# Kernel tuning notes

Hardware: AMD Instinct MI355X
Metric: run time of the kernel (lower is better)

The kernel has to match this reference:

```python
import jax, jax.numpy as jnp
import numpy as np

N, E, P = 50000, 1600000, 500000
IN_DIM, HID, OUT = 512, 128, 64
EPS = 1e-5


def setup_inputs() -> dict:
    key = jax.random.key(0)
    ks = jax.random.split(key, 16)
    d = {}
    d['x'] = jax.random.normal(ks[0], (N, IN_DIM), dtype=jnp.float32)
    d['ei'] = jax.random.randint(ks[1], (2, E), 0, N, dtype=jnp.int32)
    d['src'] = jax.random.randint(ks[2], (P,), 0, N, dtype=jnp.int32)
    d['dst'] = jax.random.randint(ks[3], (P,), 0, N, dtype=jnp.int32)
    # GCNConv layer 1 params
    d['W1'] = jax.random.normal(ks[4], (IN_DIM, HID), dtype=jnp.float32) / np.sqrt(IN_DIM)
    d['b1'] = jnp.zeros((HID,), jnp.float32)
    d['bn1_gamma'] = jnp.ones((HID,), jnp.float32)
    d['bn1_beta'] = jnp.zeros((HID,), jnp.float32)
    d['bn1_mean'] = jnp.zeros((HID,), jnp.float32)
    d['bn1_var'] = jnp.ones((HID,), jnp.float32)
    # GCNConv layer 2 params
    d['W2'] = jax.random.normal(ks[5], (HID, OUT), dtype=jnp.float32) / np.sqrt(HID)
    d['b2'] = jnp.zeros((OUT,), jnp.float32)
    d['bn2_gamma'] = jnp.ones((OUT,), jnp.float32)
    d['bn2_beta'] = jnp.zeros((OUT,), jnp.float32)
    d['bn2_mean'] = jnp.zeros((OUT,), jnp.float32)
    d['bn2_var'] = jnp.ones((OUT,), jnp.float32)
    # edge head MLP
    d['hW1'] = jax.random.normal(ks[6], (2 * OUT, OUT), dtype=jnp.float32) / np.sqrt(2 * OUT)
    d['hb1'] = jnp.zeros((OUT,), jnp.float32)
    d['hW2'] = jax.random.normal(ks[7], (OUT, 1), dtype=jnp.float32) / np.sqrt(OUT)
    d['hb2'] = jnp.zeros((1,), jnp.float32)
    return d


def gcn_conv(x, ei, W, b):
    """PyG-style GCNConv: add self-loops, symmetric deg^-1/2 normalization."""
    xw = x @ W  # [N, F]
    row, col = ei[0], ei[1]
    ones = jnp.ones((ei.shape[1],), x.dtype)
    deg = jax.ops.segment_sum(ones, col, num_segments=N) + 1.0  # +1 for self-loop
    dinv = jax.lax.rsqrt(deg)
    norm = dinv[row] * dinv[col]  # [E]
    agg = jax.ops.segment_sum(norm[:, None] * xw[row], col, num_segments=N)
    # self-loop contribution: dinv[i]^2 * xw[i]
    return agg + (dinv * dinv)[:, None] * xw + b


def bn_eval(x, gamma, beta, mean, var):
    return (x - mean) * jax.lax.rsqrt(var + EPS) * gamma + beta


def reference(x, ei, src, dst, W1, b1, bn1_gamma, bn1_beta, bn1_mean, bn1_var,
              W2, b2, bn2_gamma, bn2_beta, bn2_mean, bn2_var, hW1, hb1, hW2, hb2):
    h = jax.nn.relu(bn_eval(gcn_conv(x, ei, W1, b1), bn1_gamma, bn1_beta, bn1_mean, bn1_var))
    # dropout is identity in eval mode
    z = jax.nn.relu(bn_eval(gcn_conv(h, ei, W2, b2), bn2_gamma, bn2_beta, bn2_mean, bn2_var))
    pair = jnp.concatenate([z[src], z[dst]], axis=1)  # [P, 2*OUT]
    hmid = jax.nn.relu(pair @ hW1 + hb1)
    logits = hmid @ hW2 + hb2  # [P, 1]
    return jax.nn.sigmoid(logits).squeeze(-1)
```

## Files before the change

kernel.cpp:

```cpp
#include <hip/hip_runtime.h>
#include <math.h>


typedef __attribute__((ext_vector_type(8))) short short8x;
typedef __attribute__((ext_vector_type(4))) float f32x4;

__device__ __forceinline__ unsigned short f2bf(float f) {
  unsigned int u = __float_as_uint(f);
  unsigned int r = u + 0x7FFFu + ((u >> 16) & 1u);
  return (unsigned short)(r >> 16);
}
__device__ __forceinline__ float bf2f(unsigned short u) {
  return __uint_as_float(((unsigned int)u) << 16);
}


__global__ void zero_int_kernel(int* __restrict__ p, int n) {
  int i = blockIdx.x * blockDim.x + threadIdx.x;
  if (i < n) p[i] = 0;
}

__global__ __launch_bounds__(256) void binA_hist_kernel(const int* __restrict__ col,
                                                        int* __restrict__ bucket_count, int E,
                                                        int NBK) {
  __shared__ int hist[256];
  const int tid = threadIdx.x;
  hist[tid] = 0;
  __syncthreads();
  const int base = blockIdx.x * 4096;
#pragma unroll
  for (int j = 0; j < 16; ++j) {
    int i = base + j * 256 + tid;
    if (i < E) atomicAdd(&hist[((unsigned int)col[i]) >> 8], 1);
  }
  __syncthreads();
  if (tid < NBK) {
    int h = hist[tid];
    if (h) atomicAdd(&bucket_count[tid], h);
  }
}

__global__ __launch_bounds__(256) void scan_buckets_kernel(const int* __restrict__ bucket_count,
                                                           int* __restrict__ bucket_start,
                                                           int* __restrict__ bcur,
                                                           int* __restrict__ offs_n, int NBK,
                                                           int E) {
  __shared__ int ws[4];
  const int tid = threadIdx.x;
  const int lane = tid & 63;
  const int wid = tid >> 6;
  int v = (tid < NBK) ? bucket_count[tid] : 0;
  int incl = v;
#pragma unroll
  for (int d = 1; d < 64; d <<= 1) {
    int t = __shfl_up(incl, d, 64);
    if (lane >= d) incl += t;
  }
  if (lane == 63) ws[wid] = incl;
  __syncthreads();
  int woff = 0;
#pragma unroll
  for (int w = 0; w < 4; ++w)
    if (w < wid) woff += ws[w];
  int excl = woff + incl - v;
  if (tid < NBK) {
    bucket_start[tid] = excl;
    bcur[tid] = excl;
  }
  if (tid == 0) {
    bucket_start[NBK] = E;
    *offs_n = E;
  }
}

__global__ __launch_bounds__(256) void binA_scatter_kernel(const int* __restrict__ row,
                                                           const int* __restrict__ col,
                                                           int* __restrict__ bcur,
                                                           unsigned int* __restrict__ staging,
                                                           int E, int NBK) {
  __shared__ int hist[256];
  const int tid = threadIdx.x;
  hist[tid] = 0;
  __syncthreads();
  const int base = blockIdx.x * 4096;
  unsigned int payload[16];
  int bk[16];
#pragma unroll
  for (int j = 0; j < 16; ++j) {
    int i = base + j * 256 + tid;
    if (i < E) {
      unsigned int c = (unsigned int)col[i];
      unsigned int r = (unsigned int)row[i];
      payload[j] = (c << 16) | r;
      bk[j] = (int)(c >> 8);
      atomicAdd(&hist[bk[j]], 1);
    } else {
      bk[j] = -1;
    }
  }
  __syncthreads();
  if (tid < NBK) {
    int h = hist[tid];
    hist[tid] = h ? atomicAdd(&bcur[tid], h) : 0;
  }
  __syncthreads();
#pragma unroll
  for (int j = 0; j < 16; ++j) {
    if (bk[j] >= 0) {
      int p = atomicAdd(&hist[bk[j]], 1);
      staging[p] = payload[j];
    }
  }
}

__global__ __launch_bounds__(256) void binB1_kernel(const unsigned int* __restrict__ staging,
                                                    const int* __restrict__ bucket_start,
                                                    int* __restrict__ offs,
                                                    float* __restrict__ dinv, int N) {
  __shared__ int cnt[256];
  __shared__ int ws[4];
  const int b = blockIdx.x;
  const int n0 = b * 256;
  const int tid = threadIdx.x;
  cnt[tid] = 0;
  __syncthreads();
  const int s = bucket_start[b];
  const int e = bucket_start[b + 1];
  for (int t = s + tid; t < e; t += 256) {
    atomicAdd(&cnt[(staging[t] >> 16) & 255u], 1);
  }
  __syncthreads();
  const int deg = cnt[tid];
  const int lane = tid & 63;
  const int wid = tid >> 6;
  int incl = deg;
#pragma unroll
  for (int d = 1; d < 64; d <<= 1) {
    int t = __shfl_up(incl, d, 64);
    if (lane >= d) incl += t;
  }
  if (lane == 63) ws[wid] = incl;
  __syncthreads();
  int woff = 0;
#pragma unroll
  for (int w = 0; w < 4; ++w)
    if (w < wid) woff += ws[w];
  const int excl = woff + incl - deg;
  const int node = n0 + tid;
  if (node < N) {
    offs[node] = s + excl;
    dinv[node] = rsqrtf((float)deg + 1.0f);
  }
}

__global__ __launch_bounds__(512) void binB2_kernel(const unsigned int* __restrict__ staging,
                                                    const int* __restrict__ offs,
                                                    const int* __restrict__ bucket_start,
                                                    const float* __restrict__ dinv,
                                                    unsigned int* __restrict__ csr, int N) {
  __shared__ int cur[256];
  const int b = blockIdx.x;
  const int n0 = b * 256;
  const int tid = threadIdx.x;
  if (tid < 256 && n0 + tid < N) cur[tid] = offs[n0 + tid];
  __syncthreads();
  const int s = bucket_start[b];
  const int e = bucket_start[b + 1];
  for (int t = s + tid; t < e; t += 512) {
    unsigned int v = __builtin_nontemporal_load(&staging[t]);
    int cl = (int)((v >> 16) & 255u);
    unsigned int r = v & 0xFFFFu;
    unsigned int wd = f2bf(dinv[r]);
    int p = atomicAdd(&cur[cl], 1);
    csr[p] = (wd << 16) | r;
  }
}

__global__ void prep_bfrag_kernel(const float* __restrict__ W, unsigned short* __restrict__ out,
                                  int K, int N) {
  int idx = blockIdx.x * blockDim.x + threadIdx.x;
  int KS = K / 32;
  int total = (N / 16) * KS * 64;
  if (idx >= total) return;
  int lane = idx & 63;
  int t = idx >> 6;
  int ks = t % KS;
  int nt = t / KS;
  int n = nt * 16 + (lane & 15);
  int k0 = ks * 32 + (lane >> 4) * 8;
  unsigned short* o = out + (size_t)idx * 8;
#pragma unroll
  for (int j = 0; j < 8; ++j) o[j] = f2bf(W[(size_t)(k0 + j) * N + n]);
}

template <int K, int N, bool ABF16>
__global__ __launch_bounds__(256) void mfma_gemm_kernel(const void* __restrict__ Ap,
                                                        const unsigned short* __restrict__ Bfrag,
                                                        unsigned short* __restrict__ Cout, int M) {
  constexpr int KS = K / 32;
  constexpr int NT = N / 16;
  const int lane = threadIdx.x & 63;
  const int wid = threadIdx.x >> 6;
  const int quad = lane >> 4;
  const int lc = lane & 15;
  const int mbase = blockIdx.x * 128 + wid * 32;
  if (mbase >= M) return;

  f32x4 acc[2][NT];
#pragma unroll
  for (int mt = 0; mt < 2; ++mt)
#pragma unroll
    for (int nt = 0; nt < NT; ++nt) acc[mt][nt] = (f32x4){0.f, 0.f, 0.f, 0.f};

  int r0 = mbase + lc;
  int r1 = mbase + 16 + lc;
  if (r0 >= M) r0 = M - 1;
  if (r1 >= M) r1 = M - 1;

#pragma unroll
  for (int ks = 0; ks < KS; ++ks) {
    const int k0 = ks * 32 + quad * 8;
    short8x a[2];
    if constexpr (ABF16) {
      const unsigned short* A = (const unsigned short*)Ap;
      a[0] = *(const short8x*)(A + (size_t)r0 * K + k0);
      a[1] = *(const short8x*)(A + (size_t)r1 * K + k0);
    } else {
      const float* A = (const float*)Ap;
      const float4* p0 = (const float4*)(A + (size_t)r0 * K + k0);
      const float4* p1 = (const float4*)(A + (size_t)r1 * K + k0);
      float4 u0 = p0[0], v0 = p0[1];
      float4 u1 = p1[0], v1 = p1[1];
      short8x t0, t1;
      t0[0] = (short)f2bf(u0.x); t0[1] = (short)f2bf(u0.y);
      t0[2] = (short)f2bf(u0.z); t0[3] = (short)f2bf(u0.w);
      t0[4] = (short)f2bf(v0.x); t0[5] = (short)f2bf(v0.y);
      t0[6] = (short)f2bf(v0.z); t0[7] = (short)f2bf(v0.w);
      t1[0] = (short)f2bf(u1.x); t1[1] = (short)f2bf(u1.y);
      t1[2] = (short)f2bf(u1.z); t1[3] = (short)f2bf(u1.w);
      t1[4] = (short)f2bf(v1.x); t1[5] = (short)f2bf(v1.y);
      t1[6] = (short)f2bf(v1.z); t1[7] = (short)f2bf(v1.w);
      a[0] = t0;
      a[1] = t1;
    }
#pragma unroll
    for (int nt = 0; nt < NT; ++nt) {
      short8x b = *(const short8x*)(Bfrag + (((size_t)nt * KS + ks) * 64 + lane) * 8);
      acc[0][nt] = __builtin_amdgcn_mfma_f32_16x16x32_bf16(a[0], b, acc[0][nt], 0, 0, 0);
      acc[1][nt] = __builtin_amdgcn_mfma_f32_16x16x32_bf16(a[1], b, acc[1][nt], 0, 0, 0);
    }
  }

#pragma unroll
  for (int mt = 0; mt < 2; ++mt)
#pragma unroll
    for (int nt = 0; nt < NT; ++nt)
#pragma unroll
      for (int reg = 0; reg < 4; ++reg) {
        int row = mbase + mt * 16 + quad * 4 + reg;
        if (row < M) Cout[(size_t)row * N + nt * 16 + lc] = f2bf(acc[mt][nt][reg]);
      }
}

template <int F>
__global__ __launch_bounds__(256) void agg_fast_kernel(
    const unsigned short* __restrict__ xw, const int* __restrict__ offs,
    const unsigned int* __restrict__ csr, const float* __restrict__ dinv,
    const float* __restrict__ bias, const float* __restrict__ gamma,
    const float* __restrict__ beta, const float* __restrict__ mean,
    const float* __restrict__ var, unsigned short* __restrict__ out, int N) {
  constexpr int G = F / 2;
  constexpr int NPB = 256 / G;
  const int li = threadIdx.x % G;
  const int i = blockIdx.x * NPB + threadIdx.x / G;
  if (i >= N) return;
  const unsigned int* xw32 = (const unsigned int*)xw;
  const float di = dinv[i];
  const int s = offs[i], e = offs[i + 1];
  float accL = 0.f, accH = 0.f;
  int t = s;
  for (; t + 16 <= e; t += 16) {
    unsigned int ent[16];
#pragma unroll
    for (int j = 0; j < 16; ++j) ent[j] = csr[t + j];
    unsigned int gv[16];
#pragma unroll
    for (int j = 0; j < 16; ++j) gv[j] = xw32[(size_t)(ent[j] & 0xFFFFu) * G + li];
#pragma unroll
    for (int j = 0; j < 16; ++j) {
      float w = __uint_as_float(ent[j] & 0xFFFF0000u);
      accL += w * __uint_as_float(gv[j] << 16);
      accH += w * __uint_as_float(gv[j] & 0xFFFF0000u);
    }
  }
  for (; t + 4 <= e; t += 4) {
    unsigned int ent[4];
#pragma unroll
    for (int j = 0; j < 4; ++j) ent[j] = csr[t + j];
    unsigned int gv[4];
#pragma unroll
    for (int j = 0; j < 4; ++j) gv[j] = xw32[(size_t)(ent[j] & 0xFFFFu) * G + li];
#pragma unroll
    for (int j = 0; j < 4; ++j) {
      float w = __uint_as_float(ent[j] & 0xFFFF0000u);
      accL += w * __uint_as_float(gv[j] << 16);
      accH += w * __uint_as_float(gv[j] & 0xFFFF0000u);
    }
  }
  for (; t < e; ++t) {
    unsigned int ee = csr[t];
    unsigned int gv = xw32[(size_t)(ee & 0xFFFFu) * G + li];
    float w = __uint_as_float(ee & 0xFFFF0000u);
    accL += w * __uint_as_float(gv << 16);
    accH += w * __uint_as_float(gv & 0xFFFF0000u);
  }
  const int f0 = 2 * li, f1 = f0 + 1;
  unsigned int sv = xw32[(size_t)i * G + li];
  float v0 = di * accL + di * di * __uint_as_float(sv << 16) + bias[f0];
  float v1 = di * accH + di * di * __uint_as_float(sv & 0xFFFF0000u) + bias[f1];
  v0 = (v0 - mean[f0]) * rsqrtf(var[f0] + 1e-5f) * gamma[f0] + beta[f0];
  v1 = (v1 - mean[f1]) * rsqrtf(var[f1] + 1e-5f) * gamma[f1] + beta[f1];
  unsigned int packed =
      (unsigned int)f2bf(fmaxf(v0, 0.f)) | ((unsigned int)f2bf(fmaxf(v1, 0.f)) << 16);
  ((unsigned int*)out)[(size_t)i * G + li] = packed;
}

__global__ __launch_bounds__(256) void head_mfma_kernel(
    const unsigned short* __restrict__ z, const int* __restrict__ src,
    const int* __restrict__ dst, const unsigned short* __restrict__ bfragH,
    const float* __restrict__ hb1, const float* __restrict__ hw2,
    const float* __restrict__ hb2, float* __restrict__ out, int P) {
  const int lane = threadIdx.x & 63;
  const int quad = lane >> 4;
  const int lc = lane & 15;

  short8x bf[4][4];
#pragma unroll
  for (int nt = 0; nt < 4; ++nt)
#pragma unroll
    for (int ks = 0; ks < 4; ++ks)
      bf[nt][ks] = *(const short8x*)(bfragH + (((size_t)nt * 4 + ks) * 64 + lane) * 8);

  float b1v[4], w2v[4];
#pragma unroll
  for (int nt = 0; nt < 4; ++nt) {
    b1v[nt] = hb1[nt * 16 + lc];
    w2v[nt] = hw2[nt * 16 + lc];
  }
  const float bias2 = hb2[0];

  const int nchunks = (P + 15) / 16;
  const int gw = blockIdx.x * 4 + (threadIdx.x >> 6);
  const int nw = gridDim.x * 4;

  for (int ch = gw; ch < nchunks; ch += nw) {
    int p = ch * 16 + lc;
    int pc = p < P ? p : P - 1;
    int s = src[pc], d = dst[pc];
    const unsigned short* zs = z + (size_t)s * 64;
    const unsigned short* zd = z + (size_t)d * 64;
    short8x a[4];
    a[0] = *(const short8x*)(zs + quad * 8);
    a[1] = *(const short8x*)(zs + 32 + quad * 8);
    a[2] = *(const short8x*)(zd + quad * 8);
    a[3] = *(const short8x*)(zd + 32 + quad * 8);

    f32x4 acc[4];
#pragma unroll
    for (int nt = 0; nt < 4; ++nt) acc[nt] = (f32x4){0.f, 0.f, 0.f, 0.f};
#pragma unroll
    for (int nt = 0; nt < 4; ++nt)
#pragma unroll
      for (int t = 0; t < 4; ++t)
        acc[nt] = __builtin_amdgcn_mfma_f32_16x16x32_bf16(a[t], bf[nt][t], acc[nt], 0, 0, 0);

    float part[4];
#pragma unroll
    for (int reg = 0; reg < 4; ++reg) {
      float sum = 0.f;
#pragma unroll
      for (int nt = 0; nt < 4; ++nt) sum += fmaxf(acc[nt][reg] + b1v[nt], 0.f) * w2v[nt];
      part[reg] = sum;
    }
#pragma unroll
    for (int m = 1; m < 16; m <<= 1) {
#pragma unroll
      for (int reg = 0; reg < 4; ++reg) part[reg] += __shfl_xor(part[reg], m, 64);
    }
    if (lc == 0) {
      int pbase = ch * 16 + quad * 4;
      float4 o;
      o.x = 1.0f / (1.0f + __expf(-(part[0] + bias2)));
      o.y = 1.0f / (1.0f + __expf(-(part[1] + bias2)));
      o.z = 1.0f / (1.0f + __expf(-(part[2] + bias2)));
      o.w = 1.0f / (1.0f + __expf(-(part[3] + bias2)));
      if (pbase + 3 < P) {
        *(float4*)(out + pbase) = o;
      } else {
        float ov[4] = {o.x, o.y, o.z, o.w};
        for (int reg = 0; reg < 4; ++reg)
          if (pbase + reg < P) out[pbase + reg] = ov[reg];
      }
    }
  }
}


extern "C" void kernel_launch(void* const* d_in, const int* in_sizes, int n_in,
                              void* d_out, int out_size, void* d_ws, size_t ws_size,
                              hipStream_t stream) {
  const float* x = (const float*)d_in[0];
  const int* ei = (const int*)d_in[1];
  const int* src = (const int*)d_in[2];
  const int* dst = (const int*)d_in[3];
  const float* W1 = (const float*)d_in[4];
  const float* b1 = (const float*)d_in[5];
  const float* g1 = (const float*)d_in[6];
  const float* be1 = (const float*)d_in[7];
  const float* mu1 = (const float*)d_in[8];
  const float* va1 = (const float*)d_in[9];
  const float* W2 = (const float*)d_in[10];
  const float* b2 = (const float*)d_in[11];
  const float* g2 = (const float*)d_in[12];
  const float* be2 = (const float*)d_in[13];
  const float* mu2 = (const float*)d_in[14];
  const float* va2 = (const float*)d_in[15];
  const float* hW1 = (const float*)d_in[16];
  const float* hb1 = (const float*)d_in[17];
  const float* hW2 = (const float*)d_in[18];
  const float* hb2 = (const float*)d_in[19];
  float* out = (float*)d_out;

  const int N = in_sizes[0] / 512;
  const int E = in_sizes[1] / 2;
  const int P = in_sizes[2];
  const int* row = ei;
  const int* col = ei + E;
  const int NBK = (N + 255) / 256;
  const int NAB = (E + 4095) / 4096;

  char* wp = (char*)d_ws;
  auto alloc = [&](size_t bytes) {
    char* p = wp;
    wp += (bytes + 255) & ~(size_t)255;
    return p;
  };
  unsigned short* xw1 = (unsigned short*)alloc((size_t)N * 128 * 2);
  unsigned short* h = (unsigned short*)alloc((size_t)N * 128 * 2);
  unsigned short* xw2 = (unsigned short*)alloc((size_t)N * 64 * 2);
  unsigned short* z = (unsigned short*)alloc((size_t)N * 64 * 2);
  float* dinv = (float*)alloc((size_t)N * 4);
  int* offs = (int*)alloc((size_t)(N + 1) * 4);
  unsigned int* csr = (unsigned int*)alloc((size_t)E * 4);
  unsigned int* staging = (unsigned int*)alloc((size_t)E * 4);
  int* bucket_count = (int*)alloc((size_t)NBK * 4);
  int* bucket_start = (int*)alloc((size_t)(NBK + 1) * 4);
  int* bcur = (int*)alloc((size_t)NBK * 4);
  unsigned short* bfW1 = (unsigned short*)alloc(512 * 128 * 2);
  unsigned short* bfW2 = (unsigned short*)alloc(128 * 64 * 2);
  unsigned short* bfH = (unsigned short*)alloc(128 * 64 * 2);
  (void)ws_size;
  (void)n_in;
  (void)out_size;

  hipLaunchKernelGGL(zero_int_kernel, dim3((NBK + 255) / 256), dim3(256), 0, stream, bucket_count,
                     NBK);
  hipLaunchKernelGGL(binA_hist_kernel, dim3(NAB), dim3(256), 0, stream, col, bucket_count, E, NBK);
  hipLaunchKernelGGL(scan_buckets_kernel, dim3(1), dim3(256), 0, stream, bucket_count,
                     bucket_start, bcur, offs + N, NBK, E);
  hipLaunchKernelGGL(binA_scatter_kernel, dim3(NAB), dim3(256), 0, stream, row, col, bcur, staging,
                     E, NBK);
  hipLaunchKernelGGL(binB1_kernel, dim3(NBK), dim3(256), 0, stream, staging, bucket_start, offs,
                     dinv, N);
  hipLaunchKernelGGL(binB2_kernel, dim3(NBK), dim3(512), 0, stream, staging, offs, bucket_start,
                     dinv, csr, N);

  hipLaunchKernelGGL(prep_bfrag_kernel, dim3((8 * 16 * 64 + 255) / 256), dim3(256), 0, stream, W1,
                     bfW1, 512, 128);
  hipLaunchKernelGGL(prep_bfrag_kernel, dim3((4 * 4 * 64 + 255) / 256), dim3(256), 0, stream, W2,
                     bfW2, 128, 64);
  hipLaunchKernelGGL(prep_bfrag_kernel, dim3((4 * 4 * 64 + 255) / 256), dim3(256), 0, stream, hW1,
                     bfH, 128, 64);

  hipLaunchKernelGGL((mfma_gemm_kernel<512, 128, false>), dim3((N + 127) / 128), dim3(256), 0,
                     stream, x, bfW1, xw1, N);
  hipLaunchKernelGGL((agg_fast_kernel<128>), dim3((N + 3) / 4), dim3(256), 0, stream, xw1, offs,
                     csr, dinv, b1, g1, be1, mu1, va1, h, N);

  hipLaunchKernelGGL((mfma_gemm_kernel<128, 64, true>), dim3((N + 127) / 128), dim3(256), 0, stream,
                     h, bfW2, xw2, N);
  hipLaunchKernelGGL((agg_fast_kernel<64>), dim3((N + 7) / 8), dim3(256), 0, stream, xw2, offs,
                     csr, dinv, b2, g2, be2, mu2, va2, z, N);

  hipLaunchKernelGGL(head_mfma_kernel, dim3(2048), dim3(256), 0, stream, z, src, dst, bfH, hb1,
                     hW2, hb2, out, P);
}
```

Measured before the change: 387.2 us.

## Merge weight prep launches, add nontemporal loads, dual-chunk head with LDS weights

```diff
diff --git a/kernel.cpp b/kernel.cpp
--- a/kernel.cpp
+++ b/kernel.cpp
@@ -31,7 +31,7 @@
 #pragma unroll
   for (int j = 0; j < 16; ++j) {
     int i = base + j * 256 + tid;
-    if (i < E) atomicAdd(&hist[((unsigned int)col[i]) >> 8], 1);
+    if (i < E) atomicAdd(&hist[((unsigned int)__builtin_nontemporal_load(&col[i])) >> 8], 1);
   }
   __syncthreads();
   if (tid < NBK) {
@@ -89,8 +89,8 @@
   for (int j = 0; j < 16; ++j) {
     int i = base + j * 256 + tid;
     if (i < E) {
-      unsigned int c = (unsigned int)col[i];
-      unsigned int r = (unsigned int)row[i];
+      unsigned int c = (unsigned int)__builtin_nontemporal_load(&col[i]);
+      unsigned int r = (unsigned int)__builtin_nontemporal_load(&row[i]);
       payload[j] = (c << 16) | r;
       bk[j] = (int)(c >> 8);
       atomicAdd(&hist[bk[j]], 1);
@@ -176,12 +176,9 @@
   }
 }
 
-__global__ void prep_bfrag_kernel(const float* __restrict__ W, unsigned short* __restrict__ out,
-                                  int K, int N) {
-  int idx = blockIdx.x * blockDim.x + threadIdx.x;
+__device__ __forceinline__ void prep_one(const float* __restrict__ W,
+                                         unsigned short* __restrict__ out, int K, int N, int idx) {
   int KS = K / 32;
-  int total = (N / 16) * KS * 64;
-  if (idx >= total) return;
   int lane = idx & 63;
   int t = idx >> 6;
   int ks = t % KS;
@@ -191,6 +188,20 @@
   unsigned short* o = out + (size_t)idx * 8;
 #pragma unroll
   for (int j = 0; j < 8; ++j) o[j] = f2bf(W[(size_t)(k0 + j) * N + n]);
+}
+
+__global__ __launch_bounds__(256) void prep_all_kernel(
+    const float* __restrict__ W1, const float* __restrict__ W2, const float* __restrict__ H,
+    unsigned short* __restrict__ bfW1, unsigned short* __restrict__ bfW2,
+    unsigned short* __restrict__ bfH) {
+  int idx = blockIdx.x * 256 + threadIdx.x;
+  if (idx < 8192) {
+    prep_one(W1, bfW1, 512, 128, idx);
+  } else if (idx < 9216) {
+    prep_one(W2, bfW2, 128, 64, idx - 8192);
+  } else if (idx < 10240) {
+    prep_one(H, bfH, 128, 64, idx - 9216);
+  }
 }
 
 template <int K, int N, bool ABF16>
@@ -276,13 +287,14 @@
   if (i >= N) return;
   const unsigned int* xw32 = (const unsigned int*)xw;
   const float di = dinv[i];
-  const int s = offs[i], e = offs[i + 1];
+  const int s = __builtin_nontemporal_load(&offs[i]);
+  const int e = __builtin_nontemporal_load(&offs[i + 1]);
   float accL = 0.f, accH = 0.f;
   int t = s;
   for (; t + 16 <= e; t += 16) {
     unsigned int ent[16];
 #pragma unroll
-    for (int j = 0; j < 16; ++j) ent[j] = csr[t + j];
+    for (int j = 0; j < 16; ++j) ent[j] = __builtin_nontemporal_load(&csr[t + j]);
     unsigned int gv[16];
 #pragma unroll
     for (int j = 0; j < 16; ++j) gv[j] = xw32[(size_t)(ent[j] & 0xFFFFu) * G + li];
@@ -296,7 +308,7 @@
   for (; t + 4 <= e; t += 4) {
     unsigned int ent[4];
 #pragma unroll
-    for (int j = 0; j < 4; ++j) ent[j] = csr[t + j];
+    for (int j = 0; j < 4; ++j) ent[j] = __builtin_nontemporal_load(&csr[t + j]);
     unsigned int gv[4];
 #pragma unroll
     for (int j = 0; j < 4; ++j) gv[j] = xw32[(size_t)(ent[j] & 0xFFFFu) * G + li];
@@ -308,7 +320,7 @@
     }
   }
   for (; t < e; ++t) {
-    unsigned int ee = csr[t];
+    unsigned int ee = __builtin_nontemporal_load(&csr[t]);
     unsigned int gv = xw32[(size_t)(ee & 0xFFFFu) * G + li];
     float w = __uint_as_float(ee & 0xFFFF0000u);
     accL += w * __uint_as_float(gv << 16);
@@ -330,16 +342,16 @@
     const int* __restrict__ dst, const unsigned short* __restrict__ bfragH,
     const float* __restrict__ hb1, const float* __restrict__ hw2,
     const float* __restrict__ hb2, float* __restrict__ out, int P) {
-  const int lane = threadIdx.x & 63;
+  __shared__ short8x sbf[16 * 64];
+  const int tid = threadIdx.x;
+  {
+    const short8x* g = (const short8x*)bfragH;
+    for (int t = tid; t < 16 * 64; t += 256) sbf[t] = g[t];
+  }
+  __syncthreads();
+  const int lane = tid & 63;
   const int quad = lane >> 4;
   const int lc = lane & 15;
-
-  short8x bf[4][4];
-#pragma unroll
-  for (int nt = 0; nt < 4; ++nt)
-#pragma unroll
-    for (int ks = 0; ks < 4; ++ks)
-      bf[nt][ks] = *(const short8x*)(bfragH + (((size_t)nt * 4 + ks) * 64 + lane) * 8);
 
   float b1v[4], w2v[4];
 #pragma unroll
@@ -350,30 +362,21 @@
   const float bias2 = hb2[0];
 
   const int nchunks = (P + 15) / 16;
-  const int gw = blockIdx.x * 4 + (threadIdx.x >> 6);
+  const int gw = blockIdx.x * 4 + (tid >> 6);
   const int nw = gridDim.x * 4;
 
-  for (int ch = gw; ch < nchunks; ch += nw) {
+  auto load_a = [&](int ch, short8x* a) {
     int p = ch * 16 + lc;
     int pc = p < P ? p : P - 1;
     int s = src[pc], d = dst[pc];
     const unsigned short* zs = z + (size_t)s * 64;
     const unsigned short* zd = z + (size_t)d * 64;
-    short8x a[4];
     a[0] = *(const short8x*)(zs + quad * 8);
     a[1] = *(const short8x*)(zs + 32 + quad * 8);
     a[2] = *(const short8x*)(zd + quad * 8);
     a[3] = *(const short8x*)(zd + 32 + quad * 8);
-
-    f32x4 acc[4];
-#pragma unroll
-    for (int nt = 0; nt < 4; ++nt) acc[nt] = (f32x4){0.f, 0.f, 0.f, 0.f};
-#pragma unroll
-    for (int nt = 0; nt < 4; ++nt)
-#pragma unroll
-      for (int t = 0; t < 4; ++t)
-        acc[nt] = __builtin_amdgcn_mfma_f32_16x16x32_bf16(a[t], bf[nt][t], acc[nt], 0, 0, 0);
-
+  };
+  auto epilogue = [&](int ch, f32x4* acc) {
     float part[4];
 #pragma unroll
     for (int reg = 0; reg < 4; ++reg) {
@@ -402,6 +405,45 @@
           if (pbase + reg < P) out[pbase + reg] = ov[reg];
       }
     }
+  };
+
+  int ch = gw;
+  for (; ch + nw < nchunks; ch += 2 * nw) {
+    const int ch1 = ch + nw;
+    short8x a0[4], a1[4];
+    load_a(ch, a0);
+    load_a(ch1, a1);
+    f32x4 acc0[4], acc1[4];
+#pragma unroll
+    for (int nt = 0; nt < 4; ++nt) {
+      acc0[nt] = (f32x4){0.f, 0.f, 0.f, 0.f};
+      acc1[nt] = (f32x4){0.f, 0.f, 0.f, 0.f};
+    }
+#pragma unroll
+    for (int nt = 0; nt < 4; ++nt)
+#pragma unroll
+      for (int ks = 0; ks < 4; ++ks) {
+        short8x b = sbf[(nt * 4 + ks) * 64 + lane];
+        acc0[nt] = __builtin_amdgcn_mfma_f32_16x16x32_bf16(a0[ks], b, acc0[nt], 0, 0, 0);
+        acc1[nt] = __builtin_amdgcn_mfma_f32_16x16x32_bf16(a1[ks], b, acc1[nt], 0, 0, 0);
+      }
+    epilogue(ch, acc0);
+    epilogue(ch1, acc1);
+  }
+  for (; ch < nchunks; ch += nw) {
+    short8x a0[4];
+    load_a(ch, a0);
+    f32x4 acc0[4];
+#pragma unroll
+    for (int nt = 0; nt < 4; ++nt) acc0[nt] = (f32x4){0.f, 0.f, 0.f, 0.f};
+#pragma unroll
+    for (int nt = 0; nt < 4; ++nt)
+#pragma unroll
+      for (int ks = 0; ks < 4; ++ks) {
+        short8x b = sbf[(nt * 4 + ks) * 64 + lane];
+        acc0[nt] = __builtin_amdgcn_mfma_f32_16x16x32_bf16(a0[ks], b, acc0[nt], 0, 0, 0);
+      }
+    epilogue(ch, acc0);
   }
 }
 
@@ -475,12 +517,8 @@
   hipLaunchKernelGGL(binB2_kernel, dim3(NBK), dim3(512), 0, stream, staging, offs, bucket_start,
                      dinv, csr, N);
 
-  hipLaunchKernelGGL(prep_bfrag_kernel, dim3((8 * 16 * 64 + 255) / 256), dim3(256), 0, stream, W1,
-                     bfW1, 512, 128);
-  hipLaunchKernelGGL(prep_bfrag_kernel, dim3((4 * 4 * 64 + 255) / 256), dim3(256), 0, stream, W2,
-                     bfW2, 128, 64);
-  hipLaunchKernelGGL(prep_bfrag_kernel, dim3((4 * 4 * 64 + 255) / 256), dim3(256), 0, stream, hW1,
-                     bfH, 128, 64);
+  hipLaunchKernelGGL(prep_all_kernel, dim3(40), dim3(256), 0, stream, W1, W2, hW1, bfW1, bfW2,
+                     bfH);
 
   hipLaunchKernelGGL((mfma_gemm_kernel<512, 128, false>), dim3((N + 127) / 128), dim3(256), 0,
                      stream, x, bfW1, xw1, N);
```

Result: slower. 402.6 us (+4.0%).
